# Kernel tuning notes

Measured on AMD Instinct MI355X. Metric: run time of the kernel, lower is better.

The kernel has to match this reference:

```python
import jax, jax.numpy as jnp
import numpy as np

SIGMAS = jnp.asarray([1.0, 2.0, 3.0, 4.0, 5.0], dtype=jnp.float32)
B, K, D = 128, 49, 2048


def setup_inputs() -> dict:
    key = jax.random.key(0)
    k1, k2 = jax.random.split(key)
    x = jax.random.normal(k1, (B, K, D), dtype=jnp.float32)
    weight = jax.random.normal(k2, (1, K, D), dtype=jnp.float32)
    return {"x": x, "weight": weight}


def reference(x, weight):
    # distance over the 49-axis: (x[i] - W) broadcasts to (1,49,2048), sum dim=1 -> (1,2048)
    # vectorized over batch: (B,49,2048) - (1,49,2048) -> sum axis=1 -> (B,2048)
    d2 = jnp.sum((x - weight) ** 2, axis=1)  # (B, D)
    # per sigma: exp(-d2 / (2 sigma^2)) -> (S, B, D)
    inv = 1.0 / (2.0 * SIGMAS ** 2)  # (S,)
    kv = jnp.exp(-d2[None, :, :] * inv[:, None, None])  # (S, B, D)
    # repeat along the 49 axis and concat sigma-major over batch dim
    s, b, d = kv.shape
    out = jnp.broadcast_to(kv[:, :, None, :], (s, b, K, d)).reshape(s * b, K, d)
    return out
```

## Files before the change

kernel.cpp:

```cpp
#include <hip/hip_runtime.h>

#define BB 128
#define KK 49
#define DD 2048
#define SS 5
#define D2N (DD / 2)

typedef float f32x2 __attribute__((ext_vector_type(2)));

__global__ __launch_bounds__(256) void rbf_broadcast_kernel(
    const float* __restrict__ x, const float* __restrict__ w,
    float* __restrict__ out) {
  const int chunk = blockIdx.x & 3;
  const int b     = blockIdx.x >> 2;
  const int d2i   = chunk * 256 + threadIdx.x;

  const f32x2* xp = (const f32x2*)x + (size_t)b * (KK * D2N) + d2i;
  const f32x2* wp = (const f32x2*)w + d2i;

  float ax = 0.f, ay = 0.f;
#pragma unroll
  for (int k = 0; k < KK; ++k) {
    f32x2 xv = xp[(size_t)k * D2N];
    f32x2 wv = wp[(size_t)k * D2N];
    float dx = xv.x - wv.x;
    float dy = xv.y - wv.y;
    ax = fmaf(dx, dx, ax);
    ay = fmaf(dy, dy, ay);
  }

  const float inv[SS] = {0.5f, 0.125f, 1.0f / 18.0f, 0.03125f, 0.02f};

#pragma unroll
  for (int s = 0; s < SS; ++s) {
    f32x2 e;
    e.x = expf(-ax * inv[s]);
    e.y = expf(-ay * inv[s]);
    f32x2* op = (f32x2*)out + ((size_t)(s * BB + b) * KK) * D2N + d2i;
#pragma unroll
    for (int k = 0; k < KK; ++k) {
      op[(size_t)k * D2N] = e;
    }
  }
}

extern "C" void kernel_launch(void* const* d_in, const int* in_sizes, int n_in,
                              void* d_out, int out_size, void* d_ws,
                              size_t ws_size, hipStream_t stream) {
  const float* x = (const float*)d_in[0];
  const float* w = (const float*)d_in[1];
  float* out = (float*)d_out;
  dim3 grid(BB * 4);
  dim3 block(256);
  rbf_broadcast_kernel<<<grid, block, 0, stream>>>(x, w, out);
}
```

Measured before the change: 294.4 us.

## Widen to float4 and split the K reduction across two thread halves

Each thread now handles four contiguous floats with 128-bit loads and stores instead of two. The two halves of the block split the 49-step reduction (25 and 24 steps), combine partial sums through shared memory after a barrier, and then each half writes its own share of the broadcast rows. The aim is wider memory transactions and a shorter serial chain per thread, since the kernel is dominated by writing the large output. The cost is a block barrier, some shared memory, and divergent branches along the half boundary, which fall on whole waves.

```diff
diff --git a/kernel.cpp b/kernel.cpp
--- a/kernel.cpp
+++ b/kernel.cpp
@@ -4,42 +4,69 @@
 #define KK 49
 #define DD 2048
 #define SS 5
-#define D2N (DD / 2)
+#define D4 (DD / 4)
 
-typedef float f32x2 __attribute__((ext_vector_type(2)));
+typedef float f32x4 __attribute__((ext_vector_type(4)));
 
-__global__ __launch_bounds__(256) void rbf_broadcast_kernel(
+__global__ __launch_bounds__(256) void rbf_fused_kernel(
     const float* __restrict__ x, const float* __restrict__ w,
     float* __restrict__ out) {
   const int chunk = blockIdx.x & 3;
   const int b     = blockIdx.x >> 2;
-  const int d2i   = chunk * 256 + threadIdx.x;
+  const int tl    = threadIdx.x & 127;
+  const int hi    = threadIdx.x >> 7;
+  const int s4    = chunk * 128 + tl;
 
-  const f32x2* xp = (const f32x2*)x + (size_t)b * (KK * D2N) + d2i;
-  const f32x2* wp = (const f32x2*)w + d2i;
+  const f32x4* xp = (const f32x4*)x + (size_t)b * (KK * D4) + s4;
+  const f32x4* wp = (const f32x4*)w + s4;
 
-  float ax = 0.f, ay = 0.f;
+  f32x4 acc = {0.f, 0.f, 0.f, 0.f};
+  if (!hi) {
 #pragma unroll
-  for (int k = 0; k < KK; ++k) {
-    f32x2 xv = xp[(size_t)k * D2N];
-    f32x2 wv = wp[(size_t)k * D2N];
-    float dx = xv.x - wv.x;
-    float dy = xv.y - wv.y;
-    ax = fmaf(dx, dx, ax);
-    ay = fmaf(dy, dy, ay);
+    for (int k = 0; k < 25; ++k) {
+      f32x4 xv = xp[k * D4];
+      f32x4 wv = wp[k * D4];
+      f32x4 d  = xv - wv;
+      acc += d * d;
+    }
+  } else {
+#pragma unroll
+    for (int k = 25; k < 49; ++k) {
+      f32x4 xv = xp[k * D4];
+      f32x4 wv = wp[k * D4];
+      f32x4 d  = xv - wv;
+      acc += d * d;
+    }
   }
 
+  __shared__ f32x4 part[2][128];
+  part[hi][tl] = acc;
+  __syncthreads();
+  f32x4 d2 = acc + part[hi ^ 1][tl];
+
   const float inv[SS] = {0.5f, 0.125f, 1.0f / 18.0f, 0.03125f, 0.02f};
-
+  f32x4 e[SS];
 #pragma unroll
   for (int s = 0; s < SS; ++s) {
-    f32x2 e;
-    e.x = expf(-ax * inv[s]);
-    e.y = expf(-ay * inv[s]);
-    f32x2* op = (f32x2*)out + ((size_t)(s * BB + b) * KK) * D2N + d2i;
+    e[s].x = expf(-d2.x * inv[s]);
+    e[s].y = expf(-d2.y * inv[s]);
+    e[s].z = expf(-d2.z * inv[s]);
+    e[s].w = expf(-d2.w * inv[s]);
+  }
+
+  if (!hi) {
 #pragma unroll
-    for (int k = 0; k < KK; ++k) {
-      op[(size_t)k * D2N] = e;
+    for (int s = 0; s < SS; ++s) {
+      f32x4* op = (f32x4*)out + ((size_t)(s * BB + b) * KK) * D4 + s4;
+#pragma unroll
+      for (int k = 0; k < 25; ++k) op[k * D4] = e[s];
+    }
+  } else {
+#pragma unroll
+    for (int s = 0; s < SS; ++s) {
+      f32x4* op = (f32x4*)out + ((size_t)(s * BB + b) * KK) * D4 + s4;
+#pragma unroll
+      for (int k = 25; k < 49; ++k) op[k * D4] = e[s];
     }
   }
 }
@@ -50,7 +77,5 @@
   const float* x = (const float*)d_in[0];
   const float* w = (const float*)d_in[1];
   float* out = (float*)d_out;
-  dim3 grid(BB * 4);
-  dim3 block(256);
-  rbf_broadcast_kernel<<<grid, block, 0, stream>>>(x, w, out);
+  rbf_fused_kernel<<<dim3(BB * 4), dim3(256), 0, stream>>>(x, w, out);
 }
```

Result: no change. 293.6 us (-0.2%).
